# Performance work log

Hardware: AMD Instinct MI355X
Metric: run time of the kernel (lower is better)

The kernel has to match this reference:

```python
import jax, jax.numpy as jnp
import numpy as np

D_MODEL = 2048
N_HEAD = 16
HEAD_DIM = D_MODEL // N_HEAD
D_FF = 8192
SEQ = 2048
PAST = 2048
BATCH = 2
LN_EPS = 1e-5


def setup_inputs() -> dict:
    key = jax.random.key(0)
    ks = jax.random.split(key, 16)
    s = 0.02  # weight init scale
    return {
        "x": jax.random.normal(ks[0], (SEQ, BATCH, D_MODEL), jnp.float32),
        "k_cache": jax.random.normal(ks[1], (PAST, BATCH, N_HEAD, HEAD_DIM), jnp.float32),
        "v_cache": jax.random.normal(ks[2], (PAST, BATCH, N_HEAD, HEAD_DIM), jnp.float32),
        "mask": jnp.zeros((SEQ, PAST + SEQ), jnp.float32),
        "q_w": jax.random.normal(ks[3], (D_MODEL, D_MODEL), jnp.float32) * s,
        "q_b": jnp.zeros((D_MODEL,), jnp.float32),
        "k_w": jax.random.normal(ks[4], (D_MODEL, D_MODEL), jnp.float32) * s,
        "k_b": jnp.zeros((D_MODEL,), jnp.float32),
        "v_w": jax.random.normal(ks[5], (D_MODEL, D_MODEL), jnp.float32) * s,
        "v_b": jnp.zeros((D_MODEL,), jnp.float32),
        "o_w": jax.random.normal(ks[6], (D_MODEL, D_MODEL), jnp.float32) * s,
        "o_b": jnp.zeros((D_MODEL,), jnp.float32),
        "ln1_g": jnp.ones((D_MODEL,), jnp.float32),
        "ln1_b": jnp.zeros((D_MODEL,), jnp.float32),
        "ln2_g": jnp.ones((D_MODEL,), jnp.float32),
        "ln2_b": jnp.zeros((D_MODEL,), jnp.float32),
        "w1": jax.random.normal(ks[7], (D_MODEL, D_FF), jnp.float32) * s,
        "b1": jnp.zeros((D_FF,), jnp.float32),
        "w2": jax.random.normal(ks[8], (D_FF, D_MODEL), jnp.float32) * s,
        "b2": jnp.zeros((D_MODEL,), jnp.float32),
    }


def _layernorm(y, g, b):
    m = jnp.mean(y, axis=-1, keepdims=True)
    v = jnp.var(y, axis=-1, keepdims=True)  # biased var, matches torch LayerNorm
    return (y - m) * jax.lax.rsqrt(v + LN_EPS) * g + b


def reference(x, k_cache, v_cache, mask, q_w, q_b, k_w, k_b, v_w, v_b, o_w, o_b,
              ln1_g, ln1_b, ln2_g, ln2_b, w1, b1, w2, b2):
    S, B, D = x.shape
    H, hd = N_HEAD, HEAD_DIM

    x_norm = _layernorm(x, ln1_g, ln1_b)
    q = (x_norm @ q_w + q_b).reshape(S, B, H, hd)
    k = (x_norm @ k_w + k_b).reshape(S, B, H, hd)
    v = (x_norm @ v_w + v_b).reshape(S, B, H, hd)

    k_full = jnp.concatenate([k_cache, k], axis=0)  # [T,B,H,hd], T = past+S
    v_full = jnp.concatenate([v_cache, v], axis=0)

    # scores: [B,H,S,T]
    scores = jnp.einsum('sbhd,tbhd->bhst', q, k_full) / (hd ** 0.5)
    scores = scores + mask  # mask [S,T] broadcasts over B,H
    attn = jax.nn.softmax(scores, axis=-1)
    out = jnp.einsum('bhst,tbhd->sbhd', attn, v_full).reshape(S, B, D)
    x = x + out @ o_w + o_b

    h = _layernorm(x, ln2_g, ln2_b)
    x = x + jax.nn.gelu(h @ w1 + b1, approximate=False) @ w2 + b2
    return (x, k_full, v_full)
```

## Files before the change

### kernel.cpp

```cpp
#include <hip/hip_runtime.h>
#include <hip/hip_bf16.h>


typedef __bf16 bf16x8 __attribute__((ext_vector_type(8)));
typedef float f32x4 __attribute__((ext_vector_type(4)));
typedef float f32x16 __attribute__((ext_vector_type(16)));
typedef unsigned int u32;

__device__ __forceinline__ unsigned short f2bf(float f) {
  union { float f; unsigned u; } v; v.f = f;
  return (unsigned short)((v.u + 0x7FFFu + ((v.u >> 16) & 1u)) >> 16);
}

__device__ __forceinline__ float fexp2(float x) {
#if __has_builtin(__builtin_amdgcn_exp2f)
  return __builtin_amdgcn_exp2f(x);
#else
  float r;
  asm volatile("v_exp_f32 %0, %1\ns_nop 0" : "=v"(r) : "v"(x));
  return r;
#endif
}

__device__ __forceinline__ void gl16(const void* g, void* l) {
  __builtin_amdgcn_global_load_lds((__attribute__((address_space(1))) void*)g,
                                   (__attribute__((address_space(3))) void*)l,
                                   16, 0, 0);
}

__global__ __launch_bounds__(256) void ln_k(const float* __restrict__ X,
                                            const float* __restrict__ G,
                                            const float* __restrict__ Bb,
                                            unsigned short* __restrict__ Y) {
  const int row = blockIdx.x;
  const int tid = threadIdx.x;
  const float4* xr = (const float4*)(X + (size_t)row * 2048);
  const float4 xa = xr[tid], xb = xr[tid + 256];
  float s = xa.x + xa.y + xa.z + xa.w + xb.x + xb.y + xb.z + xb.w;
  float q = xa.x * xa.x + xa.y * xa.y + xa.z * xa.z + xa.w * xa.w +
            xb.x * xb.x + xb.y * xb.y + xb.z * xb.z + xb.w * xb.w;
  for (int off = 32; off; off >>= 1) {
    s += __shfl_xor(s, off);
    q += __shfl_xor(q, off);
  }
  __shared__ float red[8];
  const int wv = tid >> 6, ln = tid & 63;
  if (ln == 0) { red[wv] = s; red[4 + wv] = q; }
  __syncthreads();
  s = red[0] + red[1] + red[2] + red[3];
  q = red[4] + red[5] + red[6] + red[7];
  const float mean = s * (1.f / 2048.f);
  const float rstd = rsqrtf(q * (1.f / 2048.f) - mean * mean + 1e-5f);
  const float4 g0 = ((const float4*)G)[tid], g1 = ((const float4*)G)[tid + 256];
  const float4 b0 = ((const float4*)Bb)[tid], b1 = ((const float4*)Bb)[tid + 256];
  ushort4 o0, o1;
  o0.x = f2bf((xa.x - mean) * rstd * g0.x + b0.x);
  o0.y = f2bf((xa.y - mean) * rstd * g0.y + b0.y);
  o0.z = f2bf((xa.z - mean) * rstd * g0.z + b0.z);
  o0.w = f2bf((xa.w - mean) * rstd * g0.w + b0.w);
  o1.x = f2bf((xb.x - mean) * rstd * g1.x + b1.x);
  o1.y = f2bf((xb.y - mean) * rstd * g1.y + b1.y);
  o1.z = f2bf((xb.z - mean) * rstd * g1.z + b1.z);
  o1.w = f2bf((xb.w - mean) * rstd * g1.w + b1.w);
  ((ushort4*)(Y + (size_t)row * 2048))[tid] = o0;
  ((ushort4*)(Y + (size_t)row * 2048))[tid + 256] = o1;
}

__global__ __launch_bounds__(256) void wconvT(const float* __restrict__ W,
                                              unsigned short* __restrict__ Wt,
                                              int K, int N) {
  __shared__ float tl[32][33];
  const int k0 = blockIdx.x * 32, n0 = blockIdx.y * 32;
  const int x = threadIdx.x & 31, y = threadIdx.x >> 5;
  for (int i = 0; i < 4; ++i)
    tl[y + i * 8][x] = W[(size_t)(k0 + y + i * 8) * N + n0 + x];
  __syncthreads();
  for (int i = 0; i < 4; ++i)
    Wt[(size_t)(n0 + y + i * 8) * K + k0 + x] = f2bf(tl[x][y + i * 8]);
}

__global__ __launch_bounds__(256) void kpack(const float* __restrict__ src,
                                             unsigned short* __restrict__ dstb,
                                             float* __restrict__ dstf) {
  const size_t e = ((size_t)blockIdx.x * 256 + threadIdx.x) * 4;
  const int r = (int)(e >> 11), c = (int)(e & 2047);
  const int t = r >> 1, b = r & 1, h = c >> 7, d = c & 127;
  const float4 v = *(const float4*)(src + e);
  ushort4 o;
  o.x = f2bf(v.x); o.y = f2bf(v.y); o.z = f2bf(v.z); o.w = f2bf(v.w);
  *(ushort4*)(dstb + ((size_t)((b * 16 + h) * 4096 + t)) * 128 + d) = o;
  *(float4*)(dstf + (size_t)r * 2048 + c) = v;
}

__global__ __launch_bounds__(256) void vtrans(const float* __restrict__ src,
                                              unsigned short* __restrict__ dstb,
                                              float* __restrict__ dstf) {
  __shared__ float tl[32][33];
  const int bh = blockIdx.z;
  const int b = bh >> 4, h = bh & 15;
  const int t0 = blockIdx.x * 32, d0 = blockIdx.y * 32;
  const int x = threadIdx.x & 31, y = threadIdx.x >> 5;
  for (int i = 0; i < 4; ++i) {
    const int t = t0 + y + i * 8, d = d0 + x;
    const float v = src[((size_t)(t * 2 + b) * 16 + h) * 128 + d];
    tl[y + i * 8][x] = v;
    dstf[((size_t)(t * 2 + b) * 16 + h) * 128 + d] = v;
  }
  __syncthreads();
  for (int i = 0; i < 4; ++i) {
    const int d = d0 + y + i * 8, t = t0 + x;
    dstb[((size_t)bh * 128 + d) * 4096 + t] = f2bf(tl[x][y + i * 8]);
  }
}

__global__ __launch_bounds__(256) void mask0_k(const float* __restrict__ mask,
                                               u32* __restrict__ flags) {
  const float4* p = (const float4*)mask + (size_t)blockIdx.x * 8192 + threadIdx.x;
  int nz = 0;
#pragma unroll
  for (int i = 0; i < 32; ++i) {
    const float4 v = p[i * 256];
    nz |= (v.x != 0.f) | (v.y != 0.f) | (v.z != 0.f) | (v.w != 0.f);
  }
  const int r = __syncthreads_or(nz);
  if (threadIdx.x == 0) flags[blockIdx.x] = (u32)r;
}

template <int TAG, int EPI>
__global__ __launch_bounds__(512, 2) void gemm8p(
    const unsigned short* __restrict__ A, const unsigned short* __restrict__ Bt,
    const float* __restrict__ bias, unsigned short* __restrict__ Cb,
    int N, int K) {
  __shared__ unsigned short sA[2][256 * 64];
  __shared__ unsigned short sB[2][256 * 64];
  const int tid = threadIdx.x;
  const int wv = tid >> 6, ln = tid & 63;
  const int wm = wv >> 2, wn = wv & 3;
  const int nwg = gridDim.x;
  const int bid = blockIdx.x;
  const int wk = (bid & 7) * (nwg >> 3) + (bid >> 3);
  const int m0 = (wk & 15) * 256, n0 = (wk >> 4) * 256;
  const int NT = K >> 6, NI = NT >> 1;

  f32x4 acc[8][4] = {};
  bf16x8 af[4][2], bfr[2][2];

  auto ST = [&](int t, int which, int bb) {
    if (t >= NT) return;
    const unsigned short* G = (which < 2) ? A : Bt;
    const int base0 = ((which < 2) ? m0 : n0) + (which & 1) * 128;
    char* dst = (char*)((which < 2) ? &sA[bb][0] : &sB[bb][0]) + (which & 1) * 16384;
    const size_t kb = (size_t)t * 64;
#pragma unroll
    for (int c = 0; c < 2; ++c) {
      const int o = tid * 16 + c * 8192;
      const int row = o >> 7;
      const int cb = (o & 127) ^ ((row & 7) << 4);
      gl16((const char*)G + ((size_t)(base0 + row) * K + kb) * 2 + cb, dst + o);
    }
  };
  auto LDA = [&](int bb, int mh) {
    const char* base = (const char*)&sA[bb][0];
#pragma unroll
    for (int i = 0; i < 4; ++i) {
      const int r = wm * 128 + mh * 64 + i * 16 + (ln & 15);
#pragma unroll
      for (int kk = 0; kk < 2; ++kk) {
        int aa = (r << 7) + ((ln >> 4) << 4) + kk * 64;
        aa ^= (r & 7) << 4;
        af[i][kk] = *(const bf16x8*)(base + aa);
      }
    }
  };
  auto LDB = [&](int bb, int nh) {
    const char* base = (const char*)&sB[bb][0];
#pragma unroll
    for (int j = 0; j < 2; ++j) {
      const int r = wn * 64 + nh * 32 + j * 16 + (ln & 15);
#pragma unroll
      for (int kk = 0; kk < 2; ++kk) {
        int aa = (r << 7) + ((ln >> 4) << 4) + kk * 64;
        aa ^= (r & 7) << 4;
        bfr[j][kk] = *(const bf16x8*)(base + aa);
      }
    }
  };
  auto MM = [&](int mh, int nh) {
    __builtin_amdgcn_s_setprio(1);
#pragma unroll
    for (int i = 0; i < 4; ++i)
#pragma unroll
      for (int j = 0; j < 2; ++j)
#pragma unroll
        for (int kk = 0; kk < 2; ++kk)
          acc[mh * 4 + i][nh * 2 + j] = __builtin_amdgcn_mfma_f32_16x16x32_bf16(
              af[i][kk], bfr[j][kk], acc[mh * 4 + i][nh * 2 + j], 0, 0, 0);
    __builtin_amdgcn_s_setprio(0);
  };
#define BAR() __builtin_amdgcn_s_barrier()
#define VM2() asm volatile("s_waitcnt vmcnt(2)" ::: "memory")
#define VM0() asm volatile("s_waitcnt vmcnt(0)" ::: "memory")

  ST(0, 0, 0); ST(0, 1, 0); ST(0, 2, 0); ST(0, 3, 0); ST(1, 0, 1);
  VM2();
  BAR();

#pragma unroll 1
  for (int it = 0; it < NI; ++it) {
    const int t1 = 2 * it + 1, t2 = 2 * it + 2, t3 = 2 * it + 3;
    const bool lastit = (it == NI - 1);
    LDA(0, 0); LDB(0, 0); ST(t1, 1, 1); BAR(); MM(0, 0); BAR();
    LDB(0, 1);            ST(t1, 2, 1); BAR(); MM(0, 1); BAR();
    LDA(0, 1);            ST(t1, 3, 1); BAR(); MM(1, 1); BAR();
    LDB(0, 0);            ST(t2, 0, 0); BAR(); MM(1, 0);
    if (lastit) VM0(); else VM2();
    BAR();
    LDA(1, 0); LDB(1, 0); ST(t2, 1, 0); BAR(); MM(0, 0); BAR();
    LDB(1, 1);            ST(t2, 2, 0); BAR(); MM(0, 1); BAR();
    LDA(1, 1);            ST(t2, 3, 0); BAR(); MM(1, 1); BAR();
    LDB(1, 0);            ST(t3, 0, 1); BAR(); MM(1, 0);
    if (!lastit) VM2();
    BAR();
  }
#undef BAR
#undef VM2
#undef VM0

  const int lr = (ln >> 4) << 2, lc = ln & 15;
#pragma unroll
  for (int f = 0; f < 8; ++f) {
#pragma unroll
    for (int j = 0; j < 4; ++j) {
      const int n = n0 + wn * 64 + j * 16 + lc;
      const float bv = bias[n];
#pragma unroll
      for (int r = 0; r < 4; ++r) {
        const int m = m0 + wm * 128 + f * 16 + lr + r;
        float v = acc[f][j][r] + bv;
        v = 0.5f * v * (1.f + erff(v * 0.7071067811865476f));
        Cb[(size_t)m * N + n] = f2bf(v);
      }
    }
  }
}

template <int TAG, int EPI>
__global__ __launch_bounds__(512, 2) void gemm8n(
    const unsigned short* __restrict__ A, const unsigned short* __restrict__ Bt,
    const float* __restrict__ bias, const float* __restrict__ bias2,
    const float* __restrict__ bias3, const float* __restrict__ Rsd,
    float* __restrict__ Cf, unsigned short* __restrict__ Cb,
    float* __restrict__ of2, unsigned short* __restrict__ pb2,
    unsigned short* __restrict__ pb3, int N, int K) {
  __shared__ unsigned short sA[2][128 * 64];
  __shared__ unsigned short sB[2][256 * 64];
  const int tid = threadIdx.x;
  const int wv = tid >> 6, ln = tid & 63;
  const int wm = wv >> 2, wn = wv & 3;
  const int nwg = gridDim.x;
  const int bid = blockIdx.x;
  const int wk = (bid & 7) * (nwg >> 3) + (bid >> 3);
  const int m0 = (wk & 31) * 128, n0 = (wk >> 5) * 256;
  const int NT = K >> 6;

  f32x4 acc[4][4] = {};
  bf16x8 af[2][2], bfr[2][2];

  auto ST = [&](int t, int which, int bb) {
    if (t >= NT) return;
    const unsigned short* G = (which == 0) ? A : Bt;
    const int base0 = (which == 0) ? m0 : (which == 1 ? n0 : n0 + 128);
    char* dst = (which == 0) ? (char*)&sA[bb][0]
                             : (char*)&sB[bb][0] + (which - 1) * 16384;
    const size_t kb = (size_t)t * 64;
#pragma unroll
    for (int c = 0; c < 2; ++c) {
      const int o = tid * 16 + c * 8192;
      const int row = o >> 7;
      const int cb = (o & 127) ^ ((row & 7) << 4);
      gl16((const char*)G + ((size_t)(base0 + row) * K + kb) * 2 + cb, dst + o);
    }
  };
  auto LDA = [&](int bb, int mh) {
    const char* base = (const char*)&sA[bb][0];
#pragma unroll
    for (int i = 0; i < 2; ++i) {
      const int r = wm * 64 + mh * 32 + i * 16 + (ln & 15);
#pragma unroll
      for (int kk = 0; kk < 2; ++kk) {
        int aa = (r << 7) + ((ln >> 4) << 4) + kk * 64;
        aa ^= (r & 7) << 4;
        af[i][kk] = *(const bf16x8*)(base + aa);
      }
    }
  };
  auto LDB = [&](int bb, int nh) {
    const char* base = (const char*)&sB[bb][0];
#pragma unroll
    for (int j = 0; j < 2; ++j) {
      const int r = wn * 64 + nh * 32 + j * 16 + (ln & 15);
#pragma unroll
      for (int kk = 0; kk < 2; ++kk) {
        int aa = (r << 7) + ((ln >> 4) << 4) + kk * 64;
        aa ^= (r & 7) << 4;
        bfr[j][kk] = *(const bf16x8*)(base + aa);
      }
    }
  };
  auto MM = [&](int mh, int nh) {
    __builtin_amdgcn_s_setprio(1);
#pragma unroll
    for (int i = 0; i < 2; ++i)
#pragma unroll
      for (int j = 0; j < 2; ++j)
#pragma unroll
        for (int kk = 0; kk < 2; ++kk)
          acc[mh * 2 + i][nh * 2 + j] = __builtin_amdgcn_mfma_f32_16x16x32_bf16(
              af[i][kk], bfr[j][kk], acc[mh * 2 + i][nh * 2 + j], 0, 0, 0);
    __builtin_amdgcn_s_setprio(0);
  };
#define BAR() __builtin_amdgcn_s_barrier()
#define VM2() asm volatile("s_waitcnt vmcnt(2)" ::: "memory")
#define VM0() asm volatile("s_waitcnt vmcnt(0)" ::: "memory")

  ST(0, 0, 0); ST(0, 1, 0); ST(0, 2, 0); ST(1, 0, 1);
  VM2();
  BAR();

#pragma unroll 1
  for (int t = 0; t < NT; ++t) {
    const int cur = t & 1;
    LDA(cur, 0); LDB(cur, 0); ST(t + 1, 1, cur ^ 1); BAR(); MM(0, 0); BAR();
    LDB(cur, 1); ST(t + 1, 2, cur ^ 1); BAR(); MM(0, 1); BAR();
    LDA(cur, 1); BAR(); MM(1, 1); BAR();
    LDB(cur, 0); ST(t + 2, 0, cur); BAR(); MM(1, 0);
    if (t >= NT - 2) VM0(); else VM2();
    BAR();
  }
#undef BAR
#undef VM2
#undef VM0

  const int lr = (ln >> 4) << 2, lc = ln & 15;
  if (EPI == 0) {
    const int seg = n0 >> 11;
    const float* bp = seg == 0 ? bias : (seg == 1 ? bias2 : bias3);
#pragma unroll
    for (int i = 0; i < 4; ++i) {
#pragma unroll
      for (int j = 0; j < 4; ++j) {
        const int nn = (n0 & 2047) + wn * 64 + j * 16 + lc;
        const int h = nn >> 7, d = nn & 127;
        const float bv = bp[nn];
#pragma unroll
        for (int r = 0; r < 4; ++r) {
          const int m = m0 + wm * 64 + i * 16 + lr + r;
          const int s = m >> 1, b = m & 1;
          const float v = acc[i][j][r] + bv;
          if (seg == 0) {
            Cb[((size_t)(b * 16 + h) * 2048 + s) * 128 + d] = f2bf(v);
          } else if (seg == 1) {
            pb2[((size_t)(b * 16 + h) * 4096 + 2048 + s) * 128 + d] = f2bf(v);
            Cf[((size_t)((2048 + s) * 2 + b) * 16 + h) * 128 + d] = v;
          } else {
            pb3[((size_t)(b * 16 + h) * 128 + d) * 4096 + 2048 + s] = f2bf(v);
            of2[((size_t)((2048 + s) * 2 + b) * 16 + h) * 128 + d] = v;
          }
        }
      }
    }
  } else {
#pragma unroll
    for (int i = 0; i < 4; ++i) {
#pragma unroll
      for (int j = 0; j < 4; ++j) {
        const int n = n0 + wn * 64 + j * 16 + lc;
        const float bv = bias[n];
#pragma unroll
        for (int r = 0; r < 4; ++r) {
          const int m = m0 + wm * 64 + i * 16 + lr + r;
          const float v = acc[i][j][r] + bv + Rsd[(size_t)m * N + n];
          Cf[(size_t)m * N + n] = v;
        }
      }
    }
  }
}

__global__ __launch_bounds__(256, 2) void attn4(
    const unsigned short* __restrict__ Q,
    const unsigned short* __restrict__ Kf,
    const unsigned short* __restrict__ Vt,
    const float* __restrict__ mask,
    const u32* __restrict__ flags,
    unsigned short* __restrict__ ctx) {
  __shared__ __attribute__((aligned(16))) char smem[65536];
  const int tid = threadIdx.x;
  const int wv = tid >> 6;
  const int ln = tid & 63;
  const int q = ln & 31;
  const int hi = ln >> 5;
  const int sw = (q & 7) << 4;
  const int bh = blockIdx.y;
  const int s0w = blockIdx.x * 128 + wv * 32;

  const int mnz = __syncthreads_or((int)flags[tid]);

  bf16x8 qreg[8];
  {
    const char* qsrc = (const char*)Q +
        ((size_t)bh * 2048 + s0w + q) * 256 + (hi << 4);
#pragma unroll
    for (int kk = 0; kk < 8; ++kk) qreg[kk] = *(const bf16x8*)(qsrc + kk * 32);
  }

  const char* kp[8];
  const char* vp[4];
#pragma unroll
  for (int kk = 0; kk < 8; ++kk)
    kp[kk] = smem + (q << 8) + (((kk << 5) + (hi << 4)) ^ sw);
#pragma unroll
  for (int kk = 0; kk < 4; ++kk)
    vp[kk] = smem + 32768 + (q << 7) + (((kk << 5) + (hi << 4)) ^ sw);

  const char* Kg;
  const char* Vg;
  {
    const int oo = tid * 16;
    const int kr = oo >> 8, kc = oo & 255;
    Kg = (const char*)Kf + (size_t)bh * 4096 * 256 + (size_t)kr * 256 +
         (kc ^ ((kr & 7) << 4));
    const int vr = oo >> 7, vc = oo & 127;
    Vg = (const char*)Vt + (size_t)bh * 128 * 8192 + (size_t)vr * 8192 +
         (vc ^ ((vr & 7) << 4));
  }
  char* kdst = smem + tid * 16;
  char* vdst = smem + 32768 + tid * 16;

#define STAGE(BUF)                                             \
  do {                                                         \
    _Pragma("unroll") for (int is = 0; is < 4; ++is) {         \
      gl16(Kg + is * 4096, kdst + (BUF) + is * 4096);          \
      gl16(Vg + (size_t)is * 262144, vdst + (BUF) + is * 4096);\
    }                                                          \
    Kg += 16384; Vg += 128;                                    \
  } while (0)

  f32x16 acc[4] = {};
  float m = -1e30f, l = 0.f;
  const float KLOG = 0.127517445f;

  auto tile = [&](int BUF, int it) {
    f32x16 sc0, sc1;
    {
      f32x16 z = {};
      __builtin_amdgcn_s_setprio(1);
#pragma unroll
      for (int kk = 0; kk < 8; ++kk)
        z = __builtin_amdgcn_mfma_f32_32x32x16_bf16(
            *(const bf16x8*)(kp[kk] + BUF), qreg[kk], z, 0, 0, 0);
      sc0 = z;
    }
    {
      f32x16 z = {};
#pragma unroll
      for (int kk = 0; kk < 8; ++kk)
        z = __builtin_amdgcn_mfma_f32_32x32x16_bf16(
            *(const bf16x8*)(kp[kk] + BUF + 8192), qreg[kk], z, 0, 0, 0);
      __builtin_amdgcn_s_setprio(0);
      sc1 = z;
    }

    if (mnz) {
      const float rs = 11.313708498984761f;
#pragma unroll
      for (int r = 0; r < 16; ++r) {
        const int tt = it * 64 + ((r & 3) + ((r >> 2) << 3) + (hi << 2));
        sc0[r] = fmaf(mask[(size_t)(s0w + q) * 4096 + tt], rs, sc0[r]);
        sc1[r] = fmaf(mask[(size_t)(s0w + q) * 4096 + tt + 32], rs, sc1[r]);
      }
    }

    float pmax = sc0[0];
#pragma unroll
    for (int r = 1; r < 16; ++r) pmax = fmaxf(pmax, sc0[r]);
#pragma unroll
    for (int r = 0; r < 16; ++r) pmax = fmaxf(pmax, sc1[r]);
    pmax = fmaxf(pmax, __shfl_xor(pmax, 32));
    if (__any(pmax > m + 90.5f)) {
      const float mn = fmaxf(m, pmax);
      const float corr = fexp2((m - mn) * KLOG);
      m = mn; l *= corr;
#pragma unroll
      for (int d4 = 0; d4 < 4; ++d4)
#pragma unroll
        for (int e = 0; e < 16; ++e) acc[d4][e] *= corr;
    }
    const float mk = m * KLOG;
    float rsum = 0.f;
#pragma unroll
    for (int r = 0; r < 16; ++r) {
      const float e = fexp2(fmaf(sc0[r], KLOG, -mk));
      sc0[r] = e;
      rsum += e;
    }
#pragma unroll
    for (int r = 0; r < 16; ++r) {
      const float e = fexp2(fmaf(sc1[r], KLOG, -mk));
      sc1[r] = e;
      rsum += e;
    }
    rsum += __shfl_xor(rsum, 32);
    l += rsum;

    bf16x8 pw[4];
#pragma unroll
    for (int kk = 0; kk < 4; ++kk) {
      const int rb = (kk & 1) * 8;
      u32 w0, w1, w2, w3;
      if (kk < 2) {
        asm("v_cvt_pk_bf16_f32 %0, %1, %2" : "=v"(w0) : "v"(sc0[rb + 0]), "v"(sc0[rb + 1]));
        asm("v_cvt_pk_bf16_f32 %0, %1, %2" : "=v"(w1) : "v"(sc0[rb + 2]), "v"(sc0[rb + 3]));
        asm("v_cvt_pk_bf16_f32 %0, %1, %2" : "=v"(w2) : "v"(sc0[rb + 4]), "v"(sc0[rb + 5]));
        asm("v_cvt_pk_bf16_f32 %0, %1, %2" : "=v"(w3) : "v"(sc0[rb + 6]), "v"(sc0[rb + 7]));
      } else {
        asm("v_cvt_pk_bf16_f32 %0, %1, %2" : "=v"(w0) : "v"(sc1[rb + 0]), "v"(sc1[rb + 1]));
        asm("v_cvt_pk_bf16_f32 %0, %1, %2" : "=v"(w1) : "v"(sc1[rb + 2]), "v"(sc1[rb + 3]));
        asm("v_cvt_pk_bf16_f32 %0, %1, %2" : "=v"(w2) : "v"(sc1[rb + 4]), "v"(sc1[rb + 5]));
        asm("v_cvt_pk_bf16_f32 %0, %1, %2" : "=v"(w3) : "v"(sc1[rb + 6]), "v"(sc1[rb + 7]));
      }
      asm("v_permlane32_swap_b32 %0, %1" : "+v"(w0), "+v"(w2));
      asm("v_permlane32_swap_b32 %0, %1" : "+v"(w1), "+v"(w3));
      union { u32 u[4]; bf16x8 b; } pk;
      pk.u[0] = w0; pk.u[1] = w1; pk.u[2] = w2; pk.u[3] = w3;
      pw[kk] = pk.b;
    }

#pragma unroll
    for (int d4 = 0; d4 < 4; ++d4) {
      __builtin_amdgcn_s_setprio(1);
#pragma unroll
      for (int kk = 0; kk < 4; ++kk)
        acc[d4] = __builtin_amdgcn_mfma_f32_32x32x16_bf16(
            *(const bf16x8*)(vp[kk] + BUF + d4 * 4096), pw[kk], acc[d4], 0, 0, 0);
      __builtin_amdgcn_s_setprio(0);
    }
  };

  STAGE(0);
#pragma unroll 1
  for (int it2 = 0; it2 < 32; ++it2) {
    __syncthreads();
    STAGE(16384);
    tile(0, 2 * it2);
    __syncthreads();
    if (it2 < 31) STAGE(0);
    tile(16384, 2 * it2 + 1);
  }
#undef STAGE

  const float inv = 1.f / l;
  const int b = bh >> 4, h = bh & 15;
  unsigned short* crow = ctx + ((size_t)(s0w + q) * 2 + b) * 2048 + h * 128;
#pragma unroll
  for (int d4 = 0; d4 < 4; ++d4)
#pragma unroll
    for (int r = 0; r < 16; ++r) {
      const int d = d4 * 32 + (r & 3) + ((r >> 2) << 3) + (hi << 2);
      crow[d] = f2bf(acc[d4][r] * inv);
    }
}

extern "C" void kernel_launch(void* const* d_in, const int* in_sizes, int n_in,
                              void* d_out, int out_size, void* d_ws, size_t ws_size,
                              hipStream_t stream) {
  const float* x    = (const float*)d_in[0];
  const float* kc   = (const float*)d_in[1];
  const float* vc   = (const float*)d_in[2];
  const float* mask = (const float*)d_in[3];
  const float* q_w  = (const float*)d_in[4];
  const float* q_b  = (const float*)d_in[5];
  const float* k_w  = (const float*)d_in[6];
  const float* k_b  = (const float*)d_in[7];
  const float* v_w  = (const float*)d_in[8];
  const float* v_b  = (const float*)d_in[9];
  const float* o_w  = (const float*)d_in[10];
  const float* o_b  = (const float*)d_in[11];
  const float* ln1g = (const float*)d_in[12];
  const float* ln1b = (const float*)d_in[13];
  const float* ln2g = (const float*)d_in[14];
  const float* ln2b = (const float*)d_in[15];
  const float* w1   = (const float*)d_in[16];
  const float* b1   = (const float*)d_in[17];
  const float* w2   = (const float*)d_in[18];
  const float* b2   = (const float*)d_in[19];

  float* out_x = (float*)d_out;
  float* out_k = out_x + (size_t)8388608;
  float* out_v = out_k + (size_t)16777216;

  char* ws = (char*)d_ws;
  unsigned short* kf  = (unsigned short*)(ws);
  unsigned short* vft = (unsigned short*)(ws + 33554432);
  unsigned short* Wt  = (unsigned short*)(ws + 67108864);
  float*          x1  = (float*)(ws + 100663296);
  unsigned short* mid = (unsigned short*)ws;

  unsigned short* xn  = (unsigned short*)d_out;
  unsigned short* ctx = xn;
  unsigned short* qb  = (unsigned short*)((char*)d_out + 16777216);
  unsigned short* hn  = qb;
  u32* mflags = (u32*)((char*)d_out + 25165824);

  const dim3 b256(256);

  ln_k<<<4096, b256, 0, stream>>>(x, ln1g, ln1b, xn);
  kpack<<<8192, b256, 0, stream>>>(kc, kf, out_k);
  vtrans<<<dim3(64, 4, 32), b256, 0, stream>>>(vc, vft, out_v);
  mask0_k<<<256, b256, 0, stream>>>(mask, mflags);

  wconvT<<<dim3(64, 64), b256, 0, stream>>>(q_w, Wt, 2048, 2048);
  wconvT<<<dim3(64, 64), b256, 0, stream>>>(k_w, Wt + (size_t)2048 * 2048, 2048, 2048);
  wconvT<<<dim3(64, 64), b256, 0, stream>>>(v_w, Wt + (size_t)4096 * 2048, 2048, 2048);

  gemm8n<0, 0><<<768, dim3(512), 0, stream>>>(
      xn, Wt, q_b, k_b, v_b, nullptr, out_k, qb, out_v, kf, vft, 6144, 2048);

  attn4<<<dim3(16, 32), b256, 0, stream>>>(qb, kf, vft, mask, mflags, ctx);

  wconvT<<<dim3(64, 64), b256, 0, stream>>>(o_w, Wt, 2048, 2048);
  gemm8n<1, 1><<<256, dim3(512), 0, stream>>>(
      ctx, Wt, o_b, nullptr, nullptr, x, x1, nullptr, nullptr, nullptr, nullptr,
      2048, 2048);

  ln_k<<<4096, b256, 0, stream>>>(x1, ln2g, ln2b, hn);

  wconvT<<<dim3(64, 256), b256, 0, stream>>>(w1, Wt, 2048, 8192);
  gemm8p<2, 2><<<512, dim3(512), 0, stream>>>(hn, Wt, b1, mid, 8192, 2048);

  wconvT<<<dim3(256, 64), b256, 0, stream>>>(w2, Wt, 8192, 2048);
  gemm8n<3, 1><<<256, dim3(512), 0, stream>>>(
      mid, Wt, b2, nullptr, nullptr, x1, out_x, nullptr, nullptr, nullptr, nullptr,
      2048, 8192);
}
```

Measured before the change: 964.4 us.

## Deepen attention K/V prefetch with vmcnt waits and batch weight conversions

The attention loop now keeps two stages of K/V loads in flight. It uses explicit s_waitcnt vmcnt(8) plus raw barriers instead of __syncthreads, so global loads for the next tile overlap compute on the current one. Separately, the Q/K/V/O weight transposes are merged into one 4-slice launch, and the O-projection reads its slice at offset 6144 rows. The aim is to hide global-load latency in attention and cut kernel launch overhead. The cost is more fragile hand-managed synchronisation, and Wt must be large enough to hold four weights.

```diff
diff --git a/kernel.cpp b/kernel.cpp
--- a/kernel.cpp
+++ b/kernel.cpp
@@ -79,6 +79,24 @@
     Wt[(size_t)(n0 + y + i * 8) * K + k0 + x] = f2bf(tl[x][y + i * 8]);
 }
 
+__global__ __launch_bounds__(256) void wconvT4(const float* __restrict__ Wq,
+                                               const float* __restrict__ Wk,
+                                               const float* __restrict__ Wv,
+                                               const float* __restrict__ Wo,
+                                               unsigned short* __restrict__ Wt) {
+  __shared__ float tl[32][33];
+  const int z = blockIdx.z;
+  const float* W = z == 0 ? Wq : (z == 1 ? Wk : (z == 2 ? Wv : Wo));
+  unsigned short* dst = Wt + (size_t)z * 2048 * 2048;
+  const int k0 = blockIdx.x * 32, n0 = blockIdx.y * 32;
+  const int x = threadIdx.x & 31, y = threadIdx.x >> 5;
+  for (int i = 0; i < 4; ++i)
+    tl[y + i * 8][x] = W[(size_t)(k0 + y + i * 8) * 2048 + n0 + x];
+  __syncthreads();
+  for (int i = 0; i < 4; ++i)
+    dst[(size_t)(n0 + y + i * 8) * 2048 + k0 + x] = f2bf(tl[x][y + i * 8]);
+}
+
 __global__ __launch_bounds__(256) void kpack(const float* __restrict__ src,
                                              unsigned short* __restrict__ dstb,
                                              float* __restrict__ dstf) {
@@ -387,7 +405,7 @@
   }
 }
 
-__global__ __launch_bounds__(256, 2) void attn4(
+__global__ __launch_bounds__(256, 2) void attn5(
     const unsigned short* __restrict__ Q,
     const unsigned short* __restrict__ Kf,
     const unsigned short* __restrict__ Vt,
@@ -437,7 +455,7 @@
   char* kdst = smem + tid * 16;
   char* vdst = smem + 32768 + tid * 16;
 
-#define STAGE(BUF)                                             \
+#define STG(BUF)                                               \
   do {                                                         \
     _Pragma("unroll") for (int is = 0; is < 4; ++is) {         \
       gl16(Kg + is * 4096, kdst + (BUF) + is * 4096);          \
@@ -445,6 +463,9 @@
     }                                                          \
     Kg += 16384; Vg += 128;                                    \
   } while (0)
+#define BARR() __builtin_amdgcn_s_barrier()
+#define VMW8() asm volatile("s_waitcnt vmcnt(8)" ::: "memory")
+#define VMW0() asm volatile("s_waitcnt vmcnt(0)" ::: "memory")
 
   f32x16 acc[4] = {};
   float m = -1e30f, l = 0.f;
@@ -547,17 +568,28 @@
     }
   };
 
-  STAGE(0);
+  STG(0);
+  STG(16384);
 #pragma unroll 1
-  for (int it2 = 0; it2 < 32; ++it2) {
-    __syncthreads();
-    STAGE(16384);
+  for (int it2 = 0; it2 < 31; ++it2) {
+    VMW8(); BARR();
     tile(0, 2 * it2);
-    __syncthreads();
-    if (it2 < 31) STAGE(0);
+    BARR();
+    STG(0);
+    VMW8(); BARR();
     tile(16384, 2 * it2 + 1);
-  }
-#undef STAGE
+    BARR();
+    STG(16384);
+  }
+  VMW8(); BARR();
+  tile(0, 62);
+  BARR();
+  VMW0(); BARR();
+  tile(16384, 63);
+#undef STG
+#undef BARR
+#undef VMW8
+#undef VMW0
 
   const float inv = 1.f / l;
   const int b = bh >> 4, h = bh & 15;
@@ -619,19 +651,16 @@
   vtrans<<<dim3(64, 4, 32), b256, 0, stream>>>(vc, vft, out_v);
   mask0_k<<<256, b256, 0, stream>>>(mask, mflags);
 
-  wconvT<<<dim3(64, 64), b256, 0, stream>>>(q_w, Wt, 2048, 2048);
-  wconvT<<<dim3(64, 64), b256, 0, stream>>>(k_w, Wt + (size_t)2048 * 2048, 2048, 2048);
-  wconvT<<<dim3(64, 64), b256, 0, stream>>>(v_w, Wt + (size_t)4096 * 2048, 2048, 2048);
+  wconvT4<<<dim3(64, 64, 4), b256, 0, stream>>>(q_w, k_w, v_w, o_w, Wt);
 
   gemm8n<0, 0><<<768, dim3(512), 0, stream>>>(
       xn, Wt, q_b, k_b, v_b, nullptr, out_k, qb, out_v, kf, vft, 6144, 2048);
 
-  attn4<<<dim3(16, 32), b256, 0, stream>>>(qb, kf, vft, mask, mflags, ctx);
-
-  wconvT<<<dim3(64, 64), b256, 0, stream>>>(o_w, Wt, 2048, 2048);
+  attn5<<<dim3(16, 32), b256, 0, stream>>>(qb, kf, vft, mask, mflags, ctx);
+
   gemm8n<1, 1><<<256, dim3(512), 0, stream>>>(
-      ctx, Wt, o_b, nullptr, nullptr, x, x1, nullptr, nullptr, nullptr, nullptr,
-      2048, 2048);
+      ctx, Wt + (size_t)6144 * 2048, o_b, nullptr, nullptr, x, x1,
+      nullptr, nullptr, nullptr, nullptr, 2048, 2048);
 
   ln_k<<<4096, b256, 0, stream>>>(x1, ln2g, ln2b, hn);
 
```

After: 956.0 us. No clear change (-0.9%).
